# Kernel optimization log

Measured on AMD Instinct MI355X. Metric: run time of the kernel, lower is better.

The kernel has to match this reference:

```python
import jax, jax.numpy as jnp
import numpy as np

N, DIM, H = 4096, 768, 12
HD = DIM // H  # head_dim = 64


def setup_inputs() -> dict:
    key = jax.random.key(0)
    ks = jax.random.split(key, 7)
    std = 1.0 / np.sqrt(HD)
    return {
        "seq": jax.random.normal(ks[0], (N, DIM), dtype=jnp.float32),
        "Wq": jax.random.normal(ks[1], (H, HD, HD), dtype=jnp.float32) * std,
        "bq": jax.random.normal(ks[2], (H, HD), dtype=jnp.float32) * std,
        "Wk": jax.random.normal(ks[3], (H, HD, HD), dtype=jnp.float32) * std,
        "bk": jax.random.normal(ks[4], (H, HD), dtype=jnp.float32) * std,
        "Wv": jax.random.normal(ks[5], (H, HD, HD), dtype=jnp.float32) * std,
        "bv": jax.random.normal(ks[6], (H, HD), dtype=jnp.float32) * std,
    }


def reference(seq, Wq, bq, Wk, bk, Wv, bv):
    n = seq.shape[0]
    # split the feature dim into heads: [N, H, HD]
    s = seq.reshape(n, H, HD)
    # per-head linear projections (torch Linear: y = x W^T + b; W stored as [in,out])
    q = jnp.einsum("nhd,hde->hne", s, Wq) + bq[:, None, :]  # [H, N, HD]
    k = jnp.einsum("nhd,hde->hne", s, Wk) + bk[:, None, :]
    v = jnp.einsum("nhd,hde->hne", s, Wv) + bv[:, None, :]
    scale = 1.0 / jnp.sqrt(jnp.asarray(HD, dtype=seq.dtype))
    scores = jnp.einsum("hne,hme->hnm", q, k) * scale  # [H, N, N]
    attn = jax.nn.softmax(scores, axis=-1)
    out = jnp.einsum("hnm,hme->hne", attn, v)  # [H, N, HD]
    # hstack of per-head results == concat along features in head order
    return jnp.transpose(out, (1, 0, 2)).reshape(n, DIM)
```

## Files before the change

### kernel.cpp

```cpp
#include <hip/hip_runtime.h>
#include <stdint.h>
#include <stddef.h>

#define N   4096
#define DIM 768
#define H   12
#define HD  64

typedef __attribute__((ext_vector_type(4))) int   i32x4;
typedef __attribute__((ext_vector_type(2))) int   i32x2;
typedef __attribute__((ext_vector_type(4))) float f32x4;
typedef __attribute__((ext_vector_type(8))) short short8;

#define MFMA(acc, a, b) \
  acc = __builtin_amdgcn_mfma_f32_16x16x32_bf16(a, b, acc, 0, 0, 0)

static __device__ __forceinline__ int cvt_pk_bf16(float lo, float hi) {
  int r;
  asm("v_cvt_pk_bf16_f32 %0, %1, %2" : "=v"(r) : "v"(lo), "v"(hi));
  return r;
}

static __device__ __forceinline__ float fast_exp2(float x) {
#if __has_builtin(__builtin_amdgcn_exp2f)
  return __builtin_amdgcn_exp2f(x);
#else
  return exp2f(x);
#endif
}

static __device__ __forceinline__ short to_bf16(float x) {
  union { float f; uint32_t u; } v; v.f = x;
  uint32_t u = v.u;
  u += 0x7fffu + ((u >> 16) & 1u);
  return (short)(u >> 16);
}

__global__ __launch_bounds__(256) void proj_kernel(
    const float* __restrict__ seq,
    const float* __restrict__ Wq, const float* __restrict__ bq,
    const float* __restrict__ Wk, const float* __restrict__ bk,
    const float* __restrict__ Wv, const float* __restrict__ bv,
    short* __restrict__ Qo, short* __restrict__ Ko, short* __restrict__ Vto)
{
  __shared__ float s_tile[64][64];
  __shared__ float w_lds[3][64][64];
  const int h  = blockIdx.y;
  const int r0 = blockIdx.x * 64;
  const int t  = (int)threadIdx.x;

#pragma unroll
  for (int i = 0; i < 16; ++i) {
    const int idx = t + i * 256;
    const int r = idx >> 6, c = idx & 63;
    s_tile[r][c]   = seq[(size_t)(r0 + r) * DIM + h * HD + c];
    w_lds[0][r][c] = Wq[h * 4096 + idx];
    w_lds[1][r][c] = Wk[h * 4096 + idx];
    w_lds[2][r][c] = Wv[h * 4096 + idx];
  }
  __syncthreads();

  const int w = t >> 6, l = t & 63;
  const int rb = w * 16;
  float aq[16], ak[16], av[16];
  const float bqv = bq[h * HD + l];
  const float bkv = bk[h * HD + l];
  const float bvv = bv[h * HD + l];
#pragma unroll
  for (int r = 0; r < 16; ++r) { aq[r] = bqv; ak[r] = bkv; av[r] = bvv; }

#pragma unroll 4
  for (int d = 0; d < 64; ++d) {
    const float wq = w_lds[0][d][l];
    const float wk = w_lds[1][d][l];
    const float wv = w_lds[2][d][l];
#pragma unroll
    for (int r = 0; r < 16; ++r) {
      const float sv = s_tile[rb + r][d];
      aq[r] = fmaf(sv, wq, aq[r]);
      ak[r] = fmaf(sv, wk, ak[r]);
      av[r] = fmaf(sv, wv, av[r]);
    }
  }

  const float QSC = 0.1803368801111204f;
#pragma unroll
  for (int r = 0; r < 16; ++r) {
    const int n = r0 + rb + r;
    Qo[((size_t)h * N + n) * HD + l] = to_bf16(aq[r] * QSC);
    Ko[((size_t)h * N + n) * HD + l] = to_bf16(ak[r]);
    const int ns = (n & ~63) | ((n & 15) << 2) | ((n >> 4) & 3);
    Vto[((size_t)h * HD + l) * N + ns] = to_bf16(av[r]);
  }
}

__global__ __launch_bounds__(256) void attn_kernel(
    const short* __restrict__ Q, const short* __restrict__ K,
    const short* __restrict__ Vt, float* __restrict__ out)
{
  __shared__ __align__(16) char lds[40960];

  const int h  = blockIdx.y;
  const int q0 = blockIdx.x * 64;
  const int t  = (int)threadIdx.x;
  const int w  = t >> 6, l = t & 63, lr = l & 15, lg = l >> 4;

  char* const p_lds = lds + 32768 + w * 2048;

  const short* __restrict__ Qw = Q + ((size_t)h * N + q0 + w * 16) * HD;
  const char*  __restrict__ Kb = (const char*)(K  + (size_t)h * N * HD);
  const char*  __restrict__ Vb = (const char*)(Vt + (size_t)h * HD * N);

  short8 qf[2];
#pragma unroll
  for (int ds = 0; ds < 2; ++ds)
    qf[ds] = *(const short8*)(Qw + lr * HD + ds * 32 + lg * 8);

  f32x4 o[4];
  float lsum[4];
#pragma unroll
  for (int r = 0; r < 4; ++r) lsum[r] = 0.f;
#pragma unroll
  for (int eb = 0; eb < 4; ++eb) o[eb] = f32x4{0.f, 0.f, 0.f, 0.f};

  const int c0   = w * 2;
  const int c1   = c0 + 1;
  const int sr0  = c0 * 8 + (l >> 3);
  const int sr1  = sr0 + 8;
  const int scol = ((l & 7) * 16) ^ ((l >> 3) << 4);
  const int kdo0 = c0 * 1024 + l * 16;
  const int kdo1 = c1 * 1024 + l * 16;
  const char* const ks0 = Kb + (size_t)sr0 * 128 + scol;
  const char* const ks1 = Kb + (size_t)sr1 * 128 + scol;
  const char* const vs0 = Vb + (size_t)sr0 * (N * 2) + scol;
  const char* const vs1 = Vb + (size_t)sr1 * (N * 2) + scol;

  i32x4 rk0 = *(const i32x4*)ks0;
  i32x4 rk1 = *(const i32x4*)ks1;
  i32x4 rv0 = *(const i32x4*)vs0;
  i32x4 rv1 = *(const i32x4*)vs1;
  *(i32x4*)(lds + kdo0)        = rk0;
  *(i32x4*)(lds + kdo1)        = rk1;
  *(i32x4*)(lds + 8192 + kdo0) = rv0;
  *(i32x4*)(lds + 8192 + kdo1) = rv1;
  __syncthreads();

  for (int it = 0; it < N / 64; ++it) {
    const int  j1 = (it + 1) * 64;
    const bool pf = j1 < N;
    if (pf) {
      rk0 = *(const i32x4*)(ks0 + (size_t)j1 * 128);
      rk1 = *(const i32x4*)(ks1 + (size_t)j1 * 128);
      rv0 = *(const i32x4*)(vs0 + (size_t)j1 * 2);
      rv1 = *(const i32x4*)(vs1 + (size_t)j1 * 2);
    }
    const char* k_lds = lds + (it & 1) * 16384;
    const char* v_lds = k_lds + 8192;

    f32x4 s[4];
#pragma unroll
    for (int kb = 0; kb < 4; ++kb) {
      const int krow = kb * 16 + lr;
      const int kswz = (krow & 7) << 4;
      const char* kr = k_lds + krow * 128;
      const short8 kf0 = *(const short8*)(kr + ((lg * 16) ^ kswz));
      const short8 kf1 = *(const short8*)(kr + ((64 + lg * 16) ^ kswz));
      f32x4 acc = {0.f, 0.f, 0.f, 0.f};
      MFMA(acc, qf[0], kf0);
      MFMA(acc, qf[1], kf1);
      s[kb] = acc;
    }

#pragma unroll
    for (int kb = 0; kb < 4; ++kb)
#pragma unroll
      for (int r = 0; r < 4; ++r)
        s[kb][r] = fast_exp2(s[kb][r]);
#pragma unroll
    for (int r = 0; r < 4; ++r)
      lsum[r] += (s[0][r] + s[1][r]) + (s[2][r] + s[3][r]);

#pragma unroll
    for (int r = 0; r < 4; ++r) {
      const int prow = lg * 4 + r;
      i32x2 pw;
      pw[0] = cvt_pk_bf16(s[0][r], s[1][r]);
      pw[1] = cvt_pk_bf16(s[2][r], s[3][r]);
      *(i32x2*)(p_lds + prow * 128 + ((lr * 8) ^ ((prow & 7) << 4))) = pw;
    }
    asm volatile("" ::: "memory");

    short8 pa[2];
    {
      const int aswz = (lr & 7) << 4;
      const char* ar = p_lds + lr * 128;
      pa[0] = *(const short8*)(ar + ((lg * 16) ^ aswz));
      pa[1] = *(const short8*)(ar + ((64 + lg * 16) ^ aswz));
    }
#pragma unroll
    for (int eb = 0; eb < 4; ++eb) {
      const int vrow = eb * 16 + lr;
      const int vswz = (vrow & 7) << 4;
      const char* vr = v_lds + vrow * 128;
      const short8 vf0 = *(const short8*)(vr + ((lg * 16) ^ vswz));
      const short8 vf1 = *(const short8*)(vr + ((64 + lg * 16) ^ vswz));
      MFMA(o[eb], pa[0], vf0);
      MFMA(o[eb], pa[1], vf1);
    }

    if (pf) {
      char* const kn = lds + ((it + 1) & 1) * 16384;
      *(i32x4*)(kn + kdo0)        = rk0;
      *(i32x4*)(kn + kdo1)        = rk1;
      *(i32x4*)(kn + 8192 + kdo0) = rv0;
      *(i32x4*)(kn + 8192 + kdo1) = rv1;
    }
    __syncthreads();
  }

#pragma unroll
  for (int off = 1; off < 16; off <<= 1)
#pragma unroll
    for (int r = 0; r < 4; ++r)
      lsum[r] += __shfl_xor(lsum[r], off);
#pragma unroll
  for (int r = 0; r < 4; ++r) {
    const float inv = 1.0f / lsum[r];
    const int n = q0 + w * 16 + lg * 4 + r;
    float* orow = out + (size_t)n * DIM + h * HD;
#pragma unroll
    for (int eb = 0; eb < 4; ++eb)
      orow[eb * 16 + lr] = o[eb][r] * inv;
  }
}

extern "C" void kernel_launch(void* const* d_in, const int* in_sizes, int n_in,
                              void* d_out, int out_size, void* d_ws, size_t ws_size,
                              hipStream_t stream) {
  const float* seq = (const float*)d_in[0];
  const float* Wq  = (const float*)d_in[1];
  const float* bq  = (const float*)d_in[2];
  const float* Wk  = (const float*)d_in[3];
  const float* bk  = (const float*)d_in[4];
  const float* Wv  = (const float*)d_in[5];
  const float* bv  = (const float*)d_in[6];
  float* out = (float*)d_out;

  short* Qw  = (short*)d_ws;
  short* Kw  = Qw + (size_t)H * N * HD;
  short* Vtw = Kw + (size_t)H * N * HD;

  proj_kernel<<<dim3(N / 64, H), 256, 0, stream>>>(seq, Wq, bq, Wk, bk, Wv, bv,
                                                   Qw, Kw, Vtw);
  attn_kernel<<<dim3(N / 64, H), 256, 0, stream>>>(Qw, Kw, Vtw, out);
}
```

Baseline: 121.2 us.

## Keep P in registers via transposed QK MFMA and compute row sums with MFMA

Swaps the operands of the QK^T MFMA so the score fragments already have the register layout needed as the A operand of the PV MFMA. This removes the LDS round trip for P and the extra LDS buffer. The V^T column permutation is changed to match the new P element order. Row sums are now taken by an extra MFMA against a vector of bf16 ones instead of VALU adds plus shuffles, so the denominator is summed from bf16-rounded P values. The code uses software rounding to bf16 in place of the packed convert instruction.

```diff
diff --git a/kernel.cpp b/kernel.cpp
--- a/kernel.cpp
+++ b/kernel.cpp
@@ -8,18 +8,11 @@
 #define HD  64
 
 typedef __attribute__((ext_vector_type(4))) int   i32x4;
-typedef __attribute__((ext_vector_type(2))) int   i32x2;
 typedef __attribute__((ext_vector_type(4))) float f32x4;
 typedef __attribute__((ext_vector_type(8))) short short8;
 
 #define MFMA(acc, a, b) \
   acc = __builtin_amdgcn_mfma_f32_16x16x32_bf16(a, b, acc, 0, 0, 0)
-
-static __device__ __forceinline__ int cvt_pk_bf16(float lo, float hi) {
-  int r;
-  asm("v_cvt_pk_bf16_f32 %0, %1, %2" : "=v"(r) : "v"(lo), "v"(hi));
-  return r;
-}
 
 static __device__ __forceinline__ float fast_exp2(float x) {
 #if __has_builtin(__builtin_amdgcn_exp2f)
@@ -89,7 +82,8 @@
     const int n = r0 + rb + r;
     Qo[((size_t)h * N + n) * HD + l] = to_bf16(aq[r] * QSC);
     Ko[((size_t)h * N + n) * HD + l] = to_bf16(ak[r]);
-    const int ns = (n & ~63) | ((n & 15) << 2) | ((n >> 4) & 3);
+    const int loc = n & 63;
+    const int ns  = (n & ~63) | ((loc & 0x1C) << 1) | ((loc & 32) >> 3) | (loc & 3);
     Vto[((size_t)h * HD + l) * N + ns] = to_bf16(av[r]);
   }
 }
@@ -98,15 +92,13 @@
     const short* __restrict__ Q, const short* __restrict__ K,
     const short* __restrict__ Vt, float* __restrict__ out)
 {
-  __shared__ __align__(16) char lds[40960];
+  __shared__ __align__(16) char lds[32768];
 
   const int h  = blockIdx.y;
   const int q0 = blockIdx.x * 64;
   const int t  = (int)threadIdx.x;
   const int w  = t >> 6, l = t & 63, lr = l & 15, lg = l >> 4;
 
-  char* const p_lds = lds + 32768 + w * 2048;
-
   const short* __restrict__ Qw = Q + ((size_t)h * N + q0 + w * 16) * HD;
   const char*  __restrict__ Kb = (const char*)(K  + (size_t)h * N * HD);
   const char*  __restrict__ Vb = (const char*)(Vt + (size_t)h * HD * N);
@@ -116,12 +108,12 @@
   for (int ds = 0; ds < 2; ++ds)
     qf[ds] = *(const short8*)(Qw + lr * HD + ds * 32 + lg * 8);
 
-  f32x4 o[4];
-  float lsum[4];
-#pragma unroll
-  for (int r = 0; r < 4; ++r) lsum[r] = 0.f;
+  f32x4 o[4], o5;
+  o5 = f32x4{0.f, 0.f, 0.f, 0.f};
 #pragma unroll
   for (int eb = 0; eb < 4; ++eb) o[eb] = f32x4{0.f, 0.f, 0.f, 0.f};
+  const short8 vones = {0x3F80, 0x3F80, 0x3F80, 0x3F80,
+                        0x3F80, 0x3F80, 0x3F80, 0x3F80};
 
   const int c0   = w * 2;
   const int c1   = c0 + 1;
@@ -166,8 +158,8 @@
       const short8 kf0 = *(const short8*)(kr + ((lg * 16) ^ kswz));
       const short8 kf1 = *(const short8*)(kr + ((64 + lg * 16) ^ kswz));
       f32x4 acc = {0.f, 0.f, 0.f, 0.f};
-      MFMA(acc, qf[0], kf0);
-      MFMA(acc, qf[1], kf1);
+      MFMA(acc, kf0, qf[0]);
+      MFMA(acc, kf1, qf[1]);
       s[kb] = acc;
     }
 
@@ -176,27 +168,18 @@
 #pragma unroll
       for (int r = 0; r < 4; ++r)
         s[kb][r] = fast_exp2(s[kb][r]);
-#pragma unroll
-    for (int r = 0; r < 4; ++r)
-      lsum[r] += (s[0][r] + s[1][r]) + (s[2][r] + s[3][r]);
-
+
+    short8 pa0, pa1;
 #pragma unroll
     for (int r = 0; r < 4; ++r) {
-      const int prow = lg * 4 + r;
-      i32x2 pw;
-      pw[0] = cvt_pk_bf16(s[0][r], s[1][r]);
-      pw[1] = cvt_pk_bf16(s[2][r], s[3][r]);
-      *(i32x2*)(p_lds + prow * 128 + ((lr * 8) ^ ((prow & 7) << 4))) = pw;
-    }
-    asm volatile("" ::: "memory");
-
-    short8 pa[2];
-    {
-      const int aswz = (lr & 7) << 4;
-      const char* ar = p_lds + lr * 128;
-      pa[0] = *(const short8*)(ar + ((lg * 16) ^ aswz));
-      pa[1] = *(const short8*)(ar + ((64 + lg * 16) ^ aswz));
-    }
+      pa0[r]     = to_bf16(s[0][r]);
+      pa0[4 + r] = to_bf16(s[2][r]);
+      pa1[r]     = to_bf16(s[1][r]);
+      pa1[4 + r] = to_bf16(s[3][r]);
+    }
+
+    MFMA(o5, pa0, vones);
+    MFMA(o5, pa1, vones);
 #pragma unroll
     for (int eb = 0; eb < 4; ++eb) {
       const int vrow = eb * 16 + lr;
@@ -204,8 +187,8 @@
       const char* vr = v_lds + vrow * 128;
       const short8 vf0 = *(const short8*)(vr + ((lg * 16) ^ vswz));
       const short8 vf1 = *(const short8*)(vr + ((64 + lg * 16) ^ vswz));
-      MFMA(o[eb], pa[0], vf0);
-      MFMA(o[eb], pa[1], vf1);
+      MFMA(o[eb], pa0, vf0);
+      MFMA(o[eb], pa1, vf1);
     }
 
     if (pf) {
@@ -219,13 +202,8 @@
   }
 
 #pragma unroll
-  for (int off = 1; off < 16; off <<= 1)
-#pragma unroll
-    for (int r = 0; r < 4; ++r)
-      lsum[r] += __shfl_xor(lsum[r], off);
-#pragma unroll
   for (int r = 0; r < 4; ++r) {
-    const float inv = 1.0f / lsum[r];
+    const float inv = 1.0f / o5[r];
     const int n = q0 + w * 16 + lg * 4 + r;
     float* orow = out + (size_t)n * DIM + h * HD;
 #pragma unroll
```

After: 116.2 us. 4.2% less time.
